# Kernel tuning notes

Hardware: AMD Instinct MI355X
Metric: run time of the kernel (lower is better)

## Reference

```python
import jax, jax.numpy as jnp
import numpy as np

PATCH = (1, 5, 5)   # NN_patch_size (t, h, w)
CHUNK = 3600


def unfold3d_patches(video):
    """video: [B,C,T,H,W] -> [N, d] overlapping (1,5,5) patches, stride 1, VALID.
    d = C*1*5*5; N = B*T*(H-4)*(W-4). Element order within d is consistent
    across calls, which is all the L2 KNN + MSE math requires."""
    p = jax.lax.conv_general_dilated_patches(
        video, filter_shape=PATCH, window_strides=(1, 1, 1), padding='VALID')
    # p: [B, C*prod(PATCH), T', H', W']
    d = p.shape[1]
    return jnp.moveaxis(p, 1, -1).reshape(-1, d)


def knn_argmin(q, k):
    """Exact 1-NN under L2 (faiss IndexFlatL2 equivalent), chunked over queries."""
    kn = jnp.sum(k * k, axis=1)                      # [Nk]
    qc = q.reshape(-1, CHUNK, q.shape[1])            # [nchunks, CHUNK, d]

    def one_chunk(qb):
        qn = jnp.sum(qb * qb, axis=1, keepdims=True)  # [CHUNK,1]
        d2 = qn + kn[None, :] - 2.0 * (qb @ k.T)      # [CHUNK, Nk]
        return jnp.argmin(d2, axis=1)

    return jax.lax.map(one_chunk, qc).reshape(-1)    # [Nq]


def setup_inputs() -> dict:
    key = jax.random.key(0)
    k1, k2 = jax.random.split(key)
    shape = (1, 3, 4, 64, 64)  # [B,C,T,H,W]
    return {
        'result': jax.random.normal(k1, shape, dtype=jnp.float32),
        'valid_video': jax.random.normal(k2, shape, dtype=jnp.float32),
    }


def reference(result, valid_video):
    q = unfold3d_patches(result)        # [Nq, 75] query patches
    k = unfold3d_patches(valid_video)   # [Nk, 75] valid (key/value) patches
    idx = knn_argmin(q, k)              # [Nq] nearest valid patch per query
    nn = k[idx]                         # gather (F.embedding equivalent)
    # nn.MSELoss(reduction='sum')
    diff = q - nn
    return jnp.sum(diff * diff)
```

## Files before the change

kernel.cpp:

```cpp
#include <hip/hip_runtime.h>
#include <hip/hip_bf16.h>
#include <math.h>

typedef __attribute__((ext_vector_type(8))) short bf16x8;
typedef __attribute__((ext_vector_type(4))) float f32x4;
typedef unsigned short ushort_t;

#define NP 14400
#define NPK 14592
#define NS 4
#define NIT 57
#define TILEB 12288

__device__ __forceinline__ ushort_t f2bf(float f) {
  unsigned u = __float_as_uint(f);
  u += 0x7FFF + ((u >> 16) & 1);
  return (ushort_t)(u >> 16);
}
__device__ __forceinline__ float bf2f(ushort_t b) {
  return __uint_as_float(((unsigned)b) << 16);
}

__device__ __forceinline__ size_t kidx(int p, int d) {
  return ((size_t)(((p >> 6) * 12 + ((p >> 4) & 3) * 3 + (d >> 5)) * 64
          + ((d >> 3) & 3) * 16 + (p & 15))) * 8 + (d & 7);
}
__device__ __forceinline__ size_t qidx(int p, int d) {
  return ((size_t)(((p >> 4) * 3 + (d >> 5)) * 64
          + ((d >> 3) & 3) * 16 + (p & 15))) * 8 + (d & 7);
}

__global__ __launch_bounds__(256) void prep_kernel(
    const float* __restrict__ resv, const float* __restrict__ valv,
    ushort_t* __restrict__ Qb, ushort_t* __restrict__ Kb,
    float* __restrict__ qn, unsigned* __restrict__ rminb) {
  int w = threadIdx.x >> 6;
  int lane = threadIdx.x & 63;
  int pg = blockIdx.x * 4 + w;
  int isK = pg >= NPK;
  int p = isK ? pg - NPK : pg;

  if (p >= NP) {
    if (isK) {
      Kb[kidx(p, lane)] = 0;
      if (lane < 32)
        Kb[kidx(p, lane + 64)] = (lane == 11) ? (ushort_t)0x7F7F : (ushort_t)0;
    } else {
      Qb[qidx(p, lane)] = 0;
      if (lane < 32) Qb[qidx(p, lane + 64)] = 0;
      if (lane == 0) { qn[p] = 0.f; rminb[p] = 0xFFFFFFFFu; }
    }
    return;
  }

  const float* src = isK ? valv : resv;
  int t = p / 3600; int rem = p - t * 3600;
  int y = rem / 60;  int x = rem - y * 60;

  float v0, v1 = 0.f;
  {
    int d = lane;
    int c = d / 25; int r = d - c * 25; int dy = r / 5; int dx = r - dy * 5;
    v0 = src[((c * 4 + t) * 64 + (y + dy)) * 64 + (x + dx)];
  }
  if (lane < 11) {
    int d = lane + 64;
    int c = d / 25; int r = d - c * 25; int dy = r / 5; int dx = r - dy * 5;
    v1 = src[((c * 4 + t) * 64 + (y + dy)) * 64 + (x + dx)];
  }
  ushort_t b0 = f2bf(v0), b1 = f2bf(v1);
  float f0 = bf2f(b0), f1 = bf2f(b1);

  float sq = f0 * f0 + f1 * f1;
  #pragma unroll
  for (int off = 1; off < 64; off <<= 1) sq += __shfl_xor(sq, off, 64);

  if (isK) {
    ushort_t khi = f2bf(sq);
    ushort_t klo = f2bf(sq - bf2f(khi));
    ushort_t s1 = (lane < 11) ? b1
                : (lane == 11 ? khi : (lane == 12 ? klo : (ushort_t)0));
    Kb[kidx(p, lane)] = b0;
    if (lane < 32) Kb[kidx(p, lane + 64)] = s1;
  } else {
    ushort_t s0 = f2bf(-2.f * f0);
    ushort_t s1 = (lane < 11) ? f2bf(-2.f * f1)
                : ((lane == 11 || lane == 12) ? (ushort_t)0x3F80 : (ushort_t)0);
    Qb[qidx(p, lane)] = s0;
    if (lane < 32) Qb[qidx(p, lane + 64)] = s1;
    if (lane == 0) { qn[p] = sq; rminb[p] = 0xFFFFFFFFu; }
  }
}

__global__ __launch_bounds__(256, 2) void knn_kernel(
    const ushort_t* __restrict__ Qb, const ushort_t* __restrict__ Kb,
    unsigned* __restrict__ rminb) {
  int b = blockIdx.x;
  int lin = (b & 7) * 57 + (b >> 3);
  int ns = lin / 114, rowblk = lin - ns * 114;
  int brow = rowblk * 128;
  int lane = threadIdx.x & 63;
  int w = threadIdx.x >> 6;
  int l15 = lane & 15, l4 = lane >> 4;

  const char* gW = (const char*)Kb + (size_t)(ns * NIT) * TILEB
                   + w * 3072 + lane * 16;

  const char* Aw = (const char*)Qb + (size_t)(brow >> 4) * 3072 + lane * 16;
  bf16x8 af[8][3];
  #pragma unroll
  for (int rt = 0; rt < 8; ++rt)
    #pragma unroll
    for (int ks = 0; ks < 3; ++ks)
      af[rt][ks] = *(const bf16x8*)(Aw + (rt * 3 + ks) * 1024);

  float rmin[8][4];
  #pragma unroll
  for (int rt = 0; rt < 8; ++rt)
    #pragma unroll
    for (int j = 0; j < 4; ++j) rmin[rt][j] = INFINITY;

  const f32x4 fz = {0.f, 0.f, 0.f, 0.f};

  bf16x8 bbuf[2][3];

  auto loadB = [&](int bi, int it) {
    const char* g = gW + (size_t)it * TILEB;
    #pragma unroll
    for (int ks = 0; ks < 3; ++ks)
      bbuf[bi][ks] = *(const bf16x8*)(g + ks * 1024);
  };

  auto compute = [&](int bi) {
    f32x4 acc[8];
    {
      bf16x8 bv = bbuf[bi][0];
      #pragma unroll
      for (int rt = 0; rt < 8; ++rt)
        acc[rt] = __builtin_amdgcn_mfma_f32_16x16x32_bf16(af[rt][0], bv, fz, 0, 0, 0);
    }
    #pragma unroll
    for (int ks = 1; ks < 3; ++ks) {
      bf16x8 bv = bbuf[bi][ks];
      #pragma unroll
      for (int rt = 0; rt < 8; ++rt)
        acc[rt] = __builtin_amdgcn_mfma_f32_16x16x32_bf16(af[rt][ks], bv, acc[rt], 0, 0, 0);
    }
    #pragma unroll
    for (int rt = 0; rt < 8; ++rt)
      #pragma unroll
      for (int j = 0; j < 4; ++j)
        rmin[rt][j] = fminf(rmin[rt][j], acc[rt][j]);
  };

  loadB(0, 0);
  loadB(1, 1);

  int k = 0;
  #pragma unroll 1
  for (int tri = 0; tri < 27; ++tri, k += 2) {
    compute(0); loadB(0, k + 2);
    compute(1); loadB(1, k + 3);
  }
  compute(0); loadB(0, 56);
  compute(1);
  compute(0);

  #pragma unroll
  for (int rt = 0; rt < 8; ++rt)
    #pragma unroll
    for (int j = 0; j < 4; ++j) {
      float m = rmin[rt][j];
      m = fminf(m, __shfl_xor(m, 1, 64));
      m = fminf(m, __shfl_xor(m, 2, 64));
      m = fminf(m, __shfl_xor(m, 4, 64));
      m = fminf(m, __shfl_xor(m, 8, 64));
      if (l15 == 0) {
        unsigned bu = __float_as_uint(m);
        unsigned tu = bu ^ (unsigned)(((int)bu >> 31) | (int)0x80000000);
        atomicMin(&rminb[brow + rt * 16 + l4 * 4 + j], tu);
      }
    }
}

__global__ __launch_bounds__(64) void final1_kernel(
    const unsigned* __restrict__ rminb, const float* __restrict__ qn,
    float* __restrict__ partial) {
  int r = blockIdx.x * 64 + threadIdx.x;
  unsigned u = rminb[r];
  unsigned bu = (u & 0x80000000u) ? (u ^ 0x80000000u) : ~u;
  float val = __uint_as_float(bu) + qn[r];
  #pragma unroll
  for (int off = 32; off; off >>= 1) val += __shfl_down(val, off, 64);
  if (threadIdx.x == 0) partial[blockIdx.x] = val;
}

__global__ __launch_bounds__(256) void final2_kernel(
    const float* __restrict__ partial, float* __restrict__ out) {
  int t = threadIdx.x;
  float v = (t < 225) ? partial[t] : 0.f;
  #pragma unroll
  for (int off = 32; off; off >>= 1) v += __shfl_down(v, off, 64);
  __shared__ float s[4];
  if ((t & 63) == 0) s[t >> 6] = v;
  __syncthreads();
  if (t == 0) out[0] = s[0] + s[1] + s[2] + s[3];
}

extern "C" void kernel_launch(void* const* d_in, const int* in_sizes, int n_in,
                              void* d_out, int out_size, void* d_ws, size_t ws_size,
                              hipStream_t stream) {
  const float* resv = (const float*)d_in[0];
  const float* valv = (const float*)d_in[1];
  char* ws = (char*)d_ws;
  ushort_t* Qb      = (ushort_t*)ws;
  ushort_t* Kb      = (ushort_t*)(ws + 2801664);
  float* qn         = (float*)(ws + 5603328);
  unsigned* rminb   = (unsigned*)(ws + 5661696);
  float* partial    = (float*)(ws + 5720064);
  float* out = (float*)d_out;

  prep_kernel<<<7296, 256, 0, stream>>>(resv, valv, Qb, Kb, qn, rminb);
  knn_kernel<<<456, 256, 0, stream>>>(Qb, Kb, rminb);
  final1_kernel<<<225, 64, 0, stream>>>(rminb, qn, partial);
  final2_kernel<<<1, 256, 0, stream>>>(partial, out);
}
```

Measured before the change: 53.70 us.

## Retile KNN waves as 2x2 row/column grid and fuse final reductions

Each wave now covers 64 query rows by 32 key columns per iteration, arranged as a 2x2 grid across the block, instead of 128 rows by 16 columns. This halves the per-wave A-fragment registers and doubles the B loads per wave, giving a different register/load balance and more MFMA independence. The two final reduction kernels are merged into one single-block kernel to save a launch, at the cost of a serial loop over 14400 entries in one block.

```diff
diff --git a/kernel.cpp b/kernel.cpp
--- a/kernel.cpp
+++ b/kernel.cpp
@@ -10,7 +10,7 @@
 #define NPK 14592
 #define NS 4
 #define NIT 57
-#define TILEB 12288
+#define GRPB 12288
 
 __device__ __forceinline__ ushort_t f2bf(float f) {
   unsigned u = __float_as_uint(f);
@@ -101,56 +101,62 @@
   int brow = rowblk * 128;
   int lane = threadIdx.x & 63;
   int w = threadIdx.x >> 6;
+  int wr = w >> 1, wc = w & 1;
   int l15 = lane & 15, l4 = lane >> 4;
 
-  const char* gW = (const char*)Kb + (size_t)(ns * NIT) * TILEB
-                   + w * 3072 + lane * 16;
-
-  const char* Aw = (const char*)Qb + (size_t)(brow >> 4) * 3072 + lane * 16;
-  bf16x8 af[8][3];
-  #pragma unroll
-  for (int rt = 0; rt < 8; ++rt)
+  const char* gW = (const char*)Kb + (size_t)(ns * NIT) * GRPB
+                   + wc * 2 * 3072 + lane * 16;
+
+  const char* Aw = (const char*)Qb + (size_t)((brow + wr * 64) >> 4) * 3072
+                   + lane * 16;
+  bf16x8 af[4][3];
+  #pragma unroll
+  for (int rt = 0; rt < 4; ++rt)
     #pragma unroll
     for (int ks = 0; ks < 3; ++ks)
       af[rt][ks] = *(const bf16x8*)(Aw + (rt * 3 + ks) * 1024);
 
-  float rmin[8][4];
-  #pragma unroll
-  for (int rt = 0; rt < 8; ++rt)
+  float rmin[4][4];
+  #pragma unroll
+  for (int rt = 0; rt < 4; ++rt)
     #pragma unroll
     for (int j = 0; j < 4; ++j) rmin[rt][j] = INFINITY;
 
   const f32x4 fz = {0.f, 0.f, 0.f, 0.f};
 
-  bf16x8 bbuf[2][3];
+  bf16x8 bbuf[2][2][3];
 
   auto loadB = [&](int bi, int it) {
-    const char* g = gW + (size_t)it * TILEB;
-    #pragma unroll
-    for (int ks = 0; ks < 3; ++ks)
-      bbuf[bi][ks] = *(const bf16x8*)(g + ks * 1024);
+    const char* g = gW + (size_t)it * GRPB;
+    #pragma unroll
+    for (int cf = 0; cf < 2; ++cf)
+      #pragma unroll
+      for (int ks = 0; ks < 3; ++ks)
+        bbuf[bi][cf][ks] = *(const bf16x8*)(g + cf * 3072 + ks * 1024);
   };
 
   auto compute = [&](int bi) {
-    f32x4 acc[8];
-    {
-      bf16x8 bv = bbuf[bi][0];
-      #pragma unroll
-      for (int rt = 0; rt < 8; ++rt)
-        acc[rt] = __builtin_amdgcn_mfma_f32_16x16x32_bf16(af[rt][0], bv, fz, 0, 0, 0);
-    }
-    #pragma unroll
-    for (int ks = 1; ks < 3; ++ks) {
-      bf16x8 bv = bbuf[bi][ks];
-      #pragma unroll
-      for (int rt = 0; rt < 8; ++rt)
-        acc[rt] = __builtin_amdgcn_mfma_f32_16x16x32_bf16(af[rt][ks], bv, acc[rt], 0, 0, 0);
-    }
-    #pragma unroll
-    for (int rt = 0; rt < 8; ++rt)
+    f32x4 acc[4][2];
+    #pragma unroll
+    for (int cf = 0; cf < 2; ++cf)
+      #pragma unroll
+      for (int rt = 0; rt < 4; ++rt)
+        acc[rt][cf] = __builtin_amdgcn_mfma_f32_16x16x32_bf16(
+            af[rt][0], bbuf[bi][cf][0], fz, 0, 0, 0);
+    #pragma unroll
+    for (int ks = 1; ks < 3; ++ks)
+      #pragma unroll
+      for (int cf = 0; cf < 2; ++cf)
+        #pragma unroll
+        for (int rt = 0; rt < 4; ++rt)
+          acc[rt][cf] = __builtin_amdgcn_mfma_f32_16x16x32_bf16(
+              af[rt][ks], bbuf[bi][cf][ks], acc[rt][cf], 0, 0, 0);
+    #pragma unroll
+    for (int rt = 0; rt < 4; ++rt)
       #pragma unroll
       for (int j = 0; j < 4; ++j)
-        rmin[rt][j] = fminf(rmin[rt][j], acc[rt][j]);
+        rmin[rt][j] = fminf(rmin[rt][j],
+                            fminf(acc[rt][0][j], acc[rt][1][j]));
   };
 
   loadB(0, 0);
@@ -167,7 +173,7 @@
   compute(0);
 
   #pragma unroll
-  for (int rt = 0; rt < 8; ++rt)
+  for (int rt = 0; rt < 4; ++rt)
     #pragma unroll
     for (int j = 0; j < 4; ++j) {
       float m = rmin[rt][j];
@@ -178,33 +184,32 @@
       if (l15 == 0) {
         unsigned bu = __float_as_uint(m);
         unsigned tu = bu ^ (unsigned)(((int)bu >> 31) | (int)0x80000000);
-        atomicMin(&rminb[brow + rt * 16 + l4 * 4 + j], tu);
+        atomicMin(&rminb[brow + wr * 64 + rt * 16 + l4 * 4 + j], tu);
       }
     }
 }
 
-__global__ __launch_bounds__(64) void final1_kernel(
+__global__ __launch_bounds__(1024) void final_kernel(
     const unsigned* __restrict__ rminb, const float* __restrict__ qn,
-    float* __restrict__ partial) {
-  int r = blockIdx.x * 64 + threadIdx.x;
-  unsigned u = rminb[r];
-  unsigned bu = (u & 0x80000000u) ? (u ^ 0x80000000u) : ~u;
-  float val = __uint_as_float(bu) + qn[r];
-  #pragma unroll
-  for (int off = 32; off; off >>= 1) val += __shfl_down(val, off, 64);
-  if (threadIdx.x == 0) partial[blockIdx.x] = val;
-}
-
-__global__ __launch_bounds__(256) void final2_kernel(
-    const float* __restrict__ partial, float* __restrict__ out) {
+    float* __restrict__ out) {
   int t = threadIdx.x;
-  float v = (t < 225) ? partial[t] : 0.f;
-  #pragma unroll
-  for (int off = 32; off; off >>= 1) v += __shfl_down(v, off, 64);
-  __shared__ float s[4];
-  if ((t & 63) == 0) s[t >> 6] = v;
+  float s = 0.f;
+  for (int i = t; i < NP; i += 1024) {
+    unsigned u = rminb[i];
+    unsigned bu = (u & 0x80000000u) ? (u ^ 0x80000000u) : ~u;
+    s += __uint_as_float(bu) + qn[i];
+  }
+  #pragma unroll
+  for (int off = 32; off; off >>= 1) s += __shfl_down(s, off, 64);
+  __shared__ float red[16];
+  if ((t & 63) == 0) red[t >> 6] = s;
   __syncthreads();
-  if (t == 0) out[0] = s[0] + s[1] + s[2] + s[3];
+  if (t == 0) {
+    float tot = 0.f;
+    #pragma unroll
+    for (int i2 = 0; i2 < 16; ++i2) tot += red[i2];
+    out[0] = tot;
+  }
 }
 
 extern "C" void kernel_launch(void* const* d_in, const int* in_sizes, int n_in,
@@ -217,11 +222,9 @@
   ushort_t* Kb      = (ushort_t*)(ws + 2801664);
   float* qn         = (float*)(ws + 5603328);
   unsigned* rminb   = (unsigned*)(ws + 5661696);
-  float* partial    = (float*)(ws + 5720064);
   float* out = (float*)d_out;
 
   prep_kernel<<<7296, 256, 0, stream>>>(resv, valv, Qb, Kb, qn, rminb);
   knn_kernel<<<456, 256, 0, stream>>>(Qb, Kb, rminb);
-  final1_kernel<<<225, 64, 0, stream>>>(rminb, qn, partial);
-  final2_kernel<<<1, 256, 0, stream>>>(partial, out);
-}
+  final_kernel<<<1, 1024, 0, stream>>>(rminb, qn, out);
+}
```

Result: slower. 58.06 us (+8.1%).

## Halve KNN row tile to 64 and software-pipeline MFMA with min reduction

Applied to the files above, without the earlier changes.

The KNN kernel now covers 64 query rows per block instead of 128 and launches twice as many blocks (912), with the occupancy hint raised to 3 blocks per SM. The main loop is restructured so the MFMAs for the next key tile are issued before the fminf reduction of the previous tile's accumulators, using two accumulator sets. This is meant to fill the CUs better and hide MFMA latency behind the min reduction. In exchange every key tile is loaded twice as often overall and more atomics are issued.

```diff
diff --git a/kernel.cpp b/kernel.cpp
--- a/kernel.cpp
+++ b/kernel.cpp
@@ -92,82 +92,81 @@
   }
 }
 
-__global__ __launch_bounds__(256, 2) void knn_kernel(
+__global__ __launch_bounds__(256, 3) void knn_kernel(
     const ushort_t* __restrict__ Qb, const ushort_t* __restrict__ Kb,
     unsigned* __restrict__ rminb) {
   int b = blockIdx.x;
-  int lin = (b & 7) * 57 + (b >> 3);
-  int ns = lin / 114, rowblk = lin - ns * 114;
-  int brow = rowblk * 128;
+  int lin = (b & 7) * 114 + (b >> 3);
+  int ns = lin / 228, rowblk = lin - ns * 228;
+  int brow = rowblk * 64;
   int lane = threadIdx.x & 63;
   int w = threadIdx.x >> 6;
   int l15 = lane & 15, l4 = lane >> 4;
 
   const char* gW = (const char*)Kb + (size_t)(ns * NIT) * TILEB
                    + w * 3072 + lane * 16;
-
   const char* Aw = (const char*)Qb + (size_t)(brow >> 4) * 3072 + lane * 16;
-  bf16x8 af[8][3];
-  #pragma unroll
-  for (int rt = 0; rt < 8; ++rt)
+
+  bf16x8 af[4][3];
+  #pragma unroll
+  for (int rt = 0; rt < 4; ++rt)
     #pragma unroll
     for (int ks = 0; ks < 3; ++ks)
       af[rt][ks] = *(const bf16x8*)(Aw + (rt * 3 + ks) * 1024);
 
-  float rmin[8][4];
-  #pragma unroll
-  for (int rt = 0; rt < 8; ++rt)
+  float rmin[4][4];
+  #pragma unroll
+  for (int rt = 0; rt < 4; ++rt)
     #pragma unroll
     for (int j = 0; j < 4; ++j) rmin[rt][j] = INFINITY;
 
   const f32x4 fz = {0.f, 0.f, 0.f, 0.f};
 
-  bf16x8 bbuf[2][3];
-
-  auto loadB = [&](int bi, int it) {
+  bf16x8 bufA[3], bufB[3];
+  f32x4 accA[4], accB[4];
+
+  auto loadB = [&](bf16x8 (&bb)[3], int it) {
     const char* g = gW + (size_t)it * TILEB;
     #pragma unroll
     for (int ks = 0; ks < 3; ++ks)
-      bbuf[bi][ks] = *(const bf16x8*)(g + ks * 1024);
+      bb[ks] = *(const bf16x8*)(g + ks * 1024);
   };
 
-  auto compute = [&](int bi) {
-    f32x4 acc[8];
-    {
-      bf16x8 bv = bbuf[bi][0];
+  auto mfmaTo = [&](f32x4 (&acc)[4], const bf16x8 (&bb)[3]) {
+    #pragma unroll
+    for (int rt = 0; rt < 4; ++rt)
+      acc[rt] = __builtin_amdgcn_mfma_f32_16x16x32_bf16(af[rt][0], bb[0], fz, 0, 0, 0);
+    #pragma unroll
+    for (int ks = 1; ks < 3; ++ks)
       #pragma unroll
-      for (int rt = 0; rt < 8; ++rt)
-        acc[rt] = __builtin_amdgcn_mfma_f32_16x16x32_bf16(af[rt][0], bv, fz, 0, 0, 0);
-    }
-    #pragma unroll
-    for (int ks = 1; ks < 3; ++ks) {
-      bf16x8 bv = bbuf[bi][ks];
-      #pragma unroll
-      for (int rt = 0; rt < 8; ++rt)
-        acc[rt] = __builtin_amdgcn_mfma_f32_16x16x32_bf16(af[rt][ks], bv, acc[rt], 0, 0, 0);
-    }
-    #pragma unroll
-    for (int rt = 0; rt < 8; ++rt)
+      for (int rt = 0; rt < 4; ++rt)
+        acc[rt] = __builtin_amdgcn_mfma_f32_16x16x32_bf16(af[rt][ks], bb[ks], acc[rt], 0, 0, 0);
+  };
+
+  auto minAcc = [&](const f32x4 (&acc)[4]) {
+    #pragma unroll
+    for (int rt = 0; rt < 4; ++rt)
       #pragma unroll
       for (int j = 0; j < 4; ++j)
         rmin[rt][j] = fminf(rmin[rt][j], acc[rt][j]);
   };
 
-  loadB(0, 0);
-  loadB(1, 1);
+  loadB(bufA, 0); loadB(bufB, 1);
+  mfmaTo(accA, bufA);
+  loadB(bufA, 2);
 
   int k = 0;
   #pragma unroll 1
   for (int tri = 0; tri < 27; ++tri, k += 2) {
-    compute(0); loadB(0, k + 2);
-    compute(1); loadB(1, k + 3);
-  }
-  compute(0); loadB(0, 56);
-  compute(1);
-  compute(0);
-
-  #pragma unroll
-  for (int rt = 0; rt < 8; ++rt)
+    mfmaTo(accB, bufB); minAcc(accA); loadB(bufB, k + 3);
+    mfmaTo(accA, bufA); minAcc(accB); loadB(bufA, k + 4);
+  }
+  mfmaTo(accB, bufB); minAcc(accA);
+  mfmaTo(accA, bufA); minAcc(accB);
+  minAcc(accA);
+
+  #pragma unroll
+  for (int rt = 0; rt < 4; ++rt)
     #pragma unroll
     for (int j = 0; j < 4; ++j) {
       float m = rmin[rt][j];
@@ -221,7 +220,7 @@
   float* out = (float*)d_out;
 
   prep_kernel<<<7296, 256, 0, stream>>>(resv, valv, Qb, Kb, qn, rminb);
-  knn_kernel<<<456, 256, 0, stream>>>(Qb, Kb, rminb);
+  knn_kernel<<<912, 256, 0, stream>>>(Qb, Kb, rminb);
   final1_kernel<<<225, 64, 0, stream>>>(rminb, qn, partial);
   final2_kernel<<<1, 256, 0, stream>>>(partial, out);
 }
```

After: 56.32 us. 1.05x slower.
